# Kernel optimization log

Hardware: AMD Instinct MI355X
Metric: run time of the kernel (lower is better)

Reference implementation:

```python
import jax, jax.numpy as jnp
import numpy as np

D_IN = 1024
D_OUT = 1024
NUM_HEAD = 16
HEAD_DIM = D_OUT // NUM_HEAD
CTX = 2048


def setup_inputs() -> dict:
    key = jax.random.key(0)
    ks = jax.random.split(key, 7)
    s = 0.02
    x = jax.random.normal(ks[0], (2, CTX, D_IN), dtype=jnp.float32)
    Wq = jax.random.normal(ks[1], (D_IN, D_OUT), dtype=jnp.float32) * s
    Wk = jax.random.normal(ks[2], (D_IN, D_OUT), dtype=jnp.float32) * s
    Wv = jax.random.normal(ks[3], (D_IN, D_OUT), dtype=jnp.float32) * s
    Wo = jax.random.normal(ks[4], (D_OUT, D_OUT), dtype=jnp.float32) * s
    bo = jax.random.normal(ks[5], (D_OUT,), dtype=jnp.float32) * s
    return {"x": x, "Wq": Wq, "Wk": Wk, "Wv": Wv, "Wo": Wo, "bo": bo}


def reference(x, Wq, Wk, Wv, Wo, bo):
    B, T, _ = x.shape
    # QKV projections, split into heads: [B, H, T, hd]
    def split_heads(y):
        return y.reshape(B, T, NUM_HEAD, HEAD_DIM).transpose(0, 2, 1, 3)
    q = split_heads(x @ Wq)
    k = split_heads(x @ Wk)
    v = split_heads(x @ Wv)
    # scaled causal attention scores [B, H, T, T]
    scores = jnp.einsum("bhqd,bhkd->bhqk", q, k) / jnp.sqrt(
        jnp.asarray(HEAD_DIM, dtype=x.dtype))
    causal = jnp.tril(jnp.ones((T, T), dtype=bool))  # mask buffer triu(diag=1) -> keep lower tri
    scores = jnp.where(causal[None, None], scores, jnp.asarray(-jnp.inf, dtype=x.dtype))
    attn = jax.nn.softmax(scores, axis=-1)
    # dropout with droprate=0.0 is identity
    ctx = jnp.einsum("bhqk,bhkd->bhqd", attn, v)
    ctx = ctx.transpose(0, 2, 1, 3).reshape(B, T, D_OUT)
    return ctx @ Wo + bo
```

## Files before the change

kernel.cpp:

```cpp
#include <hip/hip_runtime.h>

typedef __bf16 bf16x8 __attribute__((ext_vector_type(8)));
typedef float f32x4 __attribute__((ext_vector_type(4)));
typedef float f32x16 __attribute__((ext_vector_type(16)));
typedef unsigned int u32x4 __attribute__((ext_vector_type(4)));

__device__ inline float bf2f(unsigned short u) {
    unsigned int x = ((unsigned int)u) << 16;
    return __builtin_bit_cast(float, x);
}
__device__ inline unsigned short f2bf(float f) {
    unsigned int x = __builtin_bit_cast(unsigned int, f);
    x += 0x7fff + ((x >> 16) & 1);
    return (unsigned short)(x >> 16);
}

__device__ __forceinline__ void gl_lds16(const unsigned short* g, unsigned short* l)
{
    __builtin_amdgcn_global_load_lds(
        (const __attribute__((address_space(1))) void*)g,
        (__attribute__((address_space(3))) void*)l, 16, 0, 0);
}

__global__ __launch_bounds__(256)
void prep(const float* __restrict__ x, unsigned short* __restrict__ xb,
          const float* __restrict__ Wq, const float* __restrict__ Wk,
          const float* __restrict__ Wv, unsigned short* __restrict__ wT)
{
    __shared__ unsigned short T[64][72];
    if (blockIdx.x < 2048) {
        const size_t i = ((size_t)blockIdx.x * 256 + threadIdx.x) * 8;
        float4 a = *reinterpret_cast<const float4*>(x + i);
        float4 b = *reinterpret_cast<const float4*>(x + i + 4);
        unsigned short t[8] = { f2bf(a.x), f2bf(a.y), f2bf(a.z), f2bf(a.w),
                                f2bf(b.x), f2bf(b.y), f2bf(b.z), f2bf(b.w) };
        *reinterpret_cast<uint4*>(xb + i) = *reinterpret_cast<uint4*>(t);
        return;
    }
    const int blk = blockIdx.x - 2048;
    const int z = blk >> 8, within = blk & 255;
    const float* W = (z == 0) ? Wq : (z == 1) ? Wk : Wv;
    unsigned short* dstBase = wT + (size_t)z * 1024 * 1024;
    const int k0 = (within >> 4) * 64, n0 = (within & 15) * 64;
    const int r = threadIdx.x >> 2, c0 = (threadIdx.x & 3) * 16;
    const float* src = W + (size_t)(k0 + r) * 1024 + n0 + c0;
    #pragma unroll
    for (int j = 0; j < 16; j += 4) {
        float4 f = *reinterpret_cast<const float4*>(src + j);
        T[r][c0 + j]     = f2bf(f.x);
        T[r][c0 + j + 1] = f2bf(f.y);
        T[r][c0 + j + 2] = f2bf(f.z);
        T[r][c0 + j + 3] = f2bf(f.w);
    }
    __syncthreads();
    unsigned short* dst = dstBase + (size_t)(n0 + r) * 1024 + k0 + c0;
    #pragma unroll
    for (int h = 0; h < 2; ++h) {
        unsigned short t8[8];
        #pragma unroll
        for (int j = 0; j < 8; ++j) t8[j] = T[c0 + h * 8 + j][r];
        *reinterpret_cast<uint4*>(dst + h * 8) = *reinterpret_cast<uint4*>(t8);
    }
}

__global__ __launch_bounds__(256)
void wconv(const float* __restrict__ W, unsigned short* __restrict__ wT)
{
    __shared__ unsigned short T[64][72];
    const int k0 = blockIdx.y * 64, n0 = blockIdx.x * 64;
    const int r = threadIdx.x >> 2, c0 = (threadIdx.x & 3) * 16;
    const float* src = W + (size_t)(k0 + r) * 1024 + n0 + c0;
    #pragma unroll
    for (int j = 0; j < 16; j += 4) {
        float4 f = *reinterpret_cast<const float4*>(src + j);
        T[r][c0 + j]     = f2bf(f.x);
        T[r][c0 + j + 1] = f2bf(f.y);
        T[r][c0 + j + 2] = f2bf(f.z);
        T[r][c0 + j + 3] = f2bf(f.w);
    }
    __syncthreads();
    unsigned short* dst = wT + (size_t)(n0 + r) * 1024 + k0 + c0;
    #pragma unroll
    for (int h = 0; h < 2; ++h) {
        unsigned short t8[8];
        #pragma unroll
        for (int j = 0; j < 8; ++j) t8[j] = T[c0 + h * 8 + j][r];
        *reinterpret_cast<uint4*>(dst + h * 8) = *reinterpret_cast<uint4*>(t8);
    }
}

template <int MODE>
__global__ __launch_bounds__(256)
void gemm128(const unsigned short* __restrict__ A,
             const unsigned short* __restrict__ BT,
             void* __restrict__ C0, void* __restrict__ C1,
             void* __restrict__ C2, const float* __restrict__ bias)
{
    __shared__ unsigned short As[128 * 32];
    __shared__ unsigned short Bs[128 * 32];

    const int tid = threadIdx.x;
    const int wave = tid >> 6, lane = tid & 63, quad = lane >> 4, l16 = lane & 15;
    const int wm = wave >> 1, wn = wave & 1;
    const int mBase = blockIdx.y * 128, nBase = blockIdx.x * 128;

    f32x4 acc[4][4] = {};

    const int srow = lane >> 2, sko = (lane & 3) * 8;

    for (int kb = 0; kb < 1024; kb += 32) {
        __syncthreads();
        #pragma unroll
        for (int j = 0; j < 2; ++j) {
            const int seg = wave * 2 + j;
            gl_lds16(A  + (size_t)(mBase + seg * 16 + srow) * 1024 + kb + sko,
                     As + seg * 512);
            gl_lds16(BT + (size_t)(nBase + seg * 16 + srow) * 1024 + kb + sko,
                     Bs + seg * 512);
        }
        __syncthreads();

        bf16x8 af[4], bf[4];
        #pragma unroll
        for (int t = 0; t < 4; ++t) {
            af[t] = *reinterpret_cast<const bf16x8*>(&As[(wm * 64 + t * 16 + l16) * 32 + quad * 8]);
            bf[t] = *reinterpret_cast<const bf16x8*>(&Bs[(wn * 64 + t * 16 + l16) * 32 + quad * 8]);
        }
        #pragma unroll
        for (int ti = 0; ti < 4; ++ti)
            #pragma unroll
            for (int tj = 0; tj < 4; ++tj)
                acc[ti][tj] = __builtin_amdgcn_mfma_f32_16x16x32_bf16(
                    af[ti], bf[tj], acc[ti][tj], 0, 0, 0);
    }

    #pragma unroll
    for (int ti = 0; ti < 4; ++ti) {
        const int row0 = mBase + wm * 64 + ti * 16 + quad * 4;
        #pragma unroll
        for (int tj = 0; tj < 4; ++tj) {
            const int col = nBase + wn * 64 + tj * 16 + l16;
            if constexpr (MODE == 0) {
                if (col < 1024) {
                    unsigned short* qb = (unsigned short*)C0;
                    #pragma unroll
                    for (int i = 0; i < 4; ++i)
                        qb[(size_t)(row0 + i) * 1024 + col] = f2bf(acc[ti][tj][i]);
                } else if (col < 2048) {
                    unsigned short* kb = (unsigned short*)C1;
                    #pragma unroll
                    for (int i = 0; i < 4; ++i)
                        kb[(size_t)(row0 + i) * 1024 + col - 1024] = f2bf(acc[ti][tj][i]);
                } else {
                    unsigned short* vT = (unsigned short*)C2;
                    unsigned short t4[4] = { f2bf(acc[ti][tj][0]), f2bf(acc[ti][tj][1]),
                                             f2bf(acc[ti][tj][2]), f2bf(acc[ti][tj][3]) };
                    *reinterpret_cast<uint2*>(&vT[(size_t)(col - 2048) * 4096 + row0]) =
                        *reinterpret_cast<uint2*>(t4);
                }
            } else {
                float* out = (float*)C0;
                const float ba = bias[col];
                #pragma unroll
                for (int i = 0; i < 4; ++i)
                    out[(size_t)(row0 + i) * 1024 + col] = acc[ti][tj][i] + ba;
            }
        }
    }
}

__global__ __launch_bounds__(256, 2)
void attn7(const unsigned short* __restrict__ q,
           const unsigned short* __restrict__ k,
           const unsigned short* __restrict__ vT,
           unsigned short* __restrict__ ctx)
{
    __shared__ unsigned short Ks[2][64 * 64];
    __shared__ unsigned short Vs[2][64 * 64];
    __shared__ float Lt[8 * 64];

    const int tid  = threadIdx.x;
    const int wave = tid >> 6, lane = tid & 63;
    const int q32 = lane & 31, hi = lane >> 5;
    const int slice = wave & 1;
    const int ks    = wave >> 1;
    const int j  = blockIdx.x;
    const int bh = blockIdx.y;
    const int b = bh >> 4, h = bh & 15;
    const int tokBase = b * 2048;
    const int colBase = h * 64;
    const int qtA = 31 - j, qtB = j;
    const int qloA = qtA * 64 + slice * 32;
    const int qloB = qtB * 64 + slice * 32;

    bf16x8 aqA[4], aqB[4];
    {
        const unsigned short* ra = q + (size_t)(tokBase + qloA + q32) * 1024 + colBase + hi * 8;
        const unsigned short* rb = q + (size_t)(tokBase + qloB + q32) * 1024 + colBase + hi * 8;
        #pragma unroll
        for (int c = 0; c < 4; ++c) {
            aqA[c] = *reinterpret_cast<const bf16x8*>(ra + c * 16);
            aqB[c] = *reinterpret_cast<const bf16x8*>(rb + c * 16);
        }
    }

    f32x16 oA[2] = {}, oB[2] = {};
    float lsA = 0.0f, lsB = 0.0f;

    const int s0 = (wave * 2 + 0) * 64 + lane;
    const int s1 = (wave * 2 + 1) * 64 + lane;
    const int r0 = s0 >> 3, sw0 = (s0 & 7) ^ (r0 & 7);
    const int r1 = s1 >> 3, sw1 = (s1 & 7) ^ (r1 & 7);
    const size_t kOff0 = (size_t)r0 * 1024 + colBase + sw0 * 8;
    const size_t kOff1 = (size_t)r1 * 1024 + colBase + sw1 * 8;
    const size_t vOff0 = (size_t)(colBase + r0) * 4096 + sw0 * 8;
    const size_t vOff1 = (size_t)(colBase + r1) * 4096 + sw1 * 8;

    auto stage = [&](int tok0, int buf) {
        gl_lds16(k  + (size_t)tok0 * 1024 + kOff0, &Ks[buf][(wave * 2 + 0) * 512]);
        gl_lds16(k  + (size_t)tok0 * 1024 + kOff1, &Ks[buf][(wave * 2 + 1) * 512]);
        gl_lds16(vT + vOff0 + tok0,                &Vs[buf][(wave * 2 + 0) * 512]);
        gl_lds16(vT + vOff1 + tok0,                &Vs[buf][(wave * 2 + 1) * 512]);
    };

    bf16x8 ak[4];
    bf16x8 bv[2][2];

    auto tile = [&](const bf16x8 (&aq)[4], f32x16 (&o)[2], float& ls,
                    int qlo, int klo) {
        if (klo > qlo + 31) return;
        f32x16 sc = (f32x16)0.0f;
        #pragma unroll
        for (int c = 0; c < 4; ++c)
            sc = __builtin_amdgcn_mfma_f32_32x32x16_bf16(ak[c], aq[c], sc, 0, 0, 0);
        float p[16];
        #pragma unroll
        for (int r = 0; r < 16; ++r) p[r] = __expf(sc[r] * 0.125f);
        if (klo + 31 > qlo) {
            #pragma unroll
            for (int r = 0; r < 16; ++r) {
                const int krow = (r & 3) + 8 * (r >> 2) + 4 * hi;
                if (klo + krow > qlo + q32) p[r] = 0.0f;
            }
        }
        #pragma unroll
        for (int r = 0; r < 16; ++r) ls += p[r];
        unsigned int pk[8];
        #pragma unroll
        for (int i = 0; i < 8; ++i)
            asm("v_cvt_pk_bf16_f32 %0, %1, %2"
                : "=v"(pk[i]) : "v"(p[2 * i]), "v"(p[2 * i + 1]));
        #pragma unroll
        for (int kc = 0; kc < 2; ++kc) {
            unsigned int x0 = pk[kc * 4 + 0], y0 = pk[kc * 4 + 2];
            unsigned int x1 = pk[kc * 4 + 1], y1 = pk[kc * 4 + 3];
            asm("v_permlane32_swap_b32 %0, %1" : "+v"(x0), "+v"(y0));
            asm("v_permlane32_swap_b32 %0, %1" : "+v"(x1), "+v"(y1));
            const u32x4 wv = { x0, x1, y0, y1 };
            const bf16x8 pa = __builtin_bit_cast(bf16x8, wv);
            #pragma unroll
            for (int dh = 0; dh < 2; ++dh)
                o[dh] = __builtin_amdgcn_mfma_f32_32x32x16_bf16(pa, bv[kc][dh], o[dh], 0, 0, 0);
        }
    };

    stage(tokBase, 0);
    __syncthreads();

    const int nkt = qtA + 1;
    int buf = 0;
    const int krowK = ks * 32 + q32;
    for (int kt = 0; kt < nkt; ++kt) {
        if (kt + 1 < nkt)
            stage(tokBase + (kt + 1) * 64, buf ^ 1);
        const unsigned short* KsB = Ks[buf];
        const unsigned short* VsB = Vs[buf];
        #pragma unroll
        for (int c = 0; c < 4; ++c) {
            const int u = c * 2 + hi;
            ak[c] = *reinterpret_cast<const bf16x8*>(
                &KsB[krowK * 64 + ((u ^ (krowK & 7)) * 8)]);
        }
        #pragma unroll
        for (int kc = 0; kc < 2; ++kc)
            #pragma unroll
            for (int dh = 0; dh < 2; ++dh) {
                const int vrow = dh * 32 + q32;
                const int u = ks * 4 + kc * 2 + hi;
                bv[kc][dh] = *reinterpret_cast<const bf16x8*>(
                    &VsB[vrow * 64 + ((u ^ (vrow & 7)) * 8)]);
            }
        const int klo = kt * 64 + ks * 32;
        tile(aqA, oA, lsA, qloA, klo);
        tile(aqB, oB, lsB, qloB, klo);
        if (kt + 1 < nkt)
            __syncthreads();
        buf ^= 1;
    }

    float* Obuf = reinterpret_cast<float*>(&Ks[0][0]);

    __syncthreads();
    Lt[(wave * 2 + 0) * 64 + lane] = lsA;
    Lt[(wave * 2 + 1) * 64 + lane] = lsB;

    auto writePartial = [&](const f32x16 (&o)[2]) {
        float* slot = Obuf + slice * 2048;
        #pragma unroll
        for (int r = 0; r < 16; ++r) {
            const int row = (r & 3) + 8 * (r >> 2) + 4 * hi;
            #pragma unroll
            for (int dh = 0; dh < 2; ++dh)
                slot[row * 64 + dh * 32 + q32] = o[dh][r];
        }
    };
    auto finalize = [&](int t, int qt, const f32x16 (&o)[2]) {
        const float lf = Lt[(slice * 2 + t) * 64 + q32]
                       + Lt[(slice * 2 + t) * 64 + 32 + q32]
                       + Lt[((slice + 2) * 2 + t) * 64 + q32]
                       + Lt[((slice + 2) * 2 + t) * 64 + 32 + q32];
        const float inv = 1.0f / lf;
        const float* slot = Obuf + slice * 2048;
        #pragma unroll
        for (int r = 0; r < 16; ++r) {
            const int row = (r & 3) + 8 * (r >> 2) + 4 * hi;
            const float invr = __shfl(inv, row);
            const size_t gr = (size_t)(tokBase + qt * 64 + slice * 32 + row) * 1024 + colBase;
            #pragma unroll
            for (int dh = 0; dh < 2; ++dh)
                ctx[gr + dh * 32 + q32] =
                    f2bf((o[dh][r] + slot[row * 64 + dh * 32 + q32]) * invr);
        }
    };

    if (ks == 1) writePartial(oA);
    __syncthreads();
    if (ks == 0) finalize(0, qtA, oA);
    __syncthreads();
    if (ks == 0) writePartial(oB);
    __syncthreads();
    if (ks == 1) finalize(1, qtB, oB);
}

extern "C" void kernel_launch(void* const* d_in, const int* in_sizes, int n_in,
                              void* d_out, int out_size, void* d_ws, size_t ws_size,
                              hipStream_t stream)
{
    const float* x  = (const float*)d_in[0];
    const float* Wq = (const float*)d_in[1];
    const float* Wk = (const float*)d_in[2];
    const float* Wv = (const float*)d_in[3];
    const float* Wo = (const float*)d_in[4];
    const float* bo = (const float*)d_in[5];
    float* out = (float*)d_out;

    unsigned short* xb     = (unsigned short*)d_ws;
    unsigned short* qb     = xb + (size_t)4096 * 1024;
    unsigned short* kb     = qb + (size_t)4096 * 1024;
    unsigned short* vT     = kb + (size_t)4096 * 1024;
    unsigned short* ctx    = xb;
    unsigned short* wqkvT  = (unsigned short*)d_out;
    unsigned short* woT    = kb;

    prep<<<2816, 256, 0, stream>>>(x, xb, Wq, Wk, Wv, wqkvT);

    gemm128<0><<<dim3(24, 32), 256, 0, stream>>>(xb, wqkvT, qb, kb, vT, nullptr);

    attn7<<<dim3(16, 32), 256, 0, stream>>>(qb, kb, vT, ctx);

    wconv<<<dim3(16, 16), 256, 0, stream>>>(Wo, woT);

    gemm128<2><<<dim3(8, 32), 256, 0, stream>>>(ctx, woT, out, nullptr, nullptr, bo);
}
```

Baseline: 183.3 us.

## Triple-buffer attention K/V staging, fold softmax scale into Q, remap blocks per XCD

The attention kernel now keeps three K/V LDS buffers with two tiles in flight. It uses explicit vmcnt waits plus a single barrier per iteration in place of two syncthreads. The 1/sqrt(d)*log2(e) scale is folded into Q during the projection GEMM epilogue so the softmax uses raw exp2. Blocks are remapped so each XCD gets a contiguous set of heads for L2 locality, and MFMA sections are wrapped in setprio. The extra buffer increases LDS use, which may affect the two-blocks-per-CU occupancy, and the hand-written vmcnt counts depend on the exact number of loads issued per stage.

```diff
diff --git a/kernel.cpp b/kernel.cpp
--- a/kernel.cpp
+++ b/kernel.cpp
@@ -5,15 +5,17 @@
 typedef float f32x16 __attribute__((ext_vector_type(16)));
 typedef unsigned int u32x4 __attribute__((ext_vector_type(4)));
 
-__device__ inline float bf2f(unsigned short u) {
-    unsigned int x = ((unsigned int)u) << 16;
-    return __builtin_bit_cast(float, x);
-}
 __device__ inline unsigned short f2bf(float f) {
     unsigned int x = __builtin_bit_cast(unsigned int, f);
     x += 0x7fff + ((x >> 16) & 1);
     return (unsigned short)(x >> 16);
 }
+
+#if __has_builtin(__builtin_amdgcn_exp2f)
+#define EXP2F(x) __builtin_amdgcn_exp2f(x)
+#else
+#define EXP2F(x) exp2f(x)
+#endif
 
 __device__ __forceinline__ void gl_lds16(const unsigned short* g, unsigned short* l)
 {
@@ -89,6 +91,8 @@
     }
 }
 
+#define QSCALE 0.18033688011112042f
+
 template <int MODE>
 __global__ __launch_bounds__(256)
 void gemm128(const unsigned short* __restrict__ A,
@@ -145,7 +149,7 @@
                     unsigned short* qb = (unsigned short*)C0;
                     #pragma unroll
                     for (int i = 0; i < 4; ++i)
-                        qb[(size_t)(row0 + i) * 1024 + col] = f2bf(acc[ti][tj][i]);
+                        qb[(size_t)(row0 + i) * 1024 + col] = f2bf(acc[ti][tj][i] * QSCALE);
                 } else if (col < 2048) {
                     unsigned short* kb = (unsigned short*)C1;
                     #pragma unroll
@@ -170,13 +174,13 @@
 }
 
 __global__ __launch_bounds__(256, 2)
-void attn7(const unsigned short* __restrict__ q,
+void attn8(const unsigned short* __restrict__ q,
            const unsigned short* __restrict__ k,
            const unsigned short* __restrict__ vT,
            unsigned short* __restrict__ ctx)
 {
-    __shared__ unsigned short Ks[2][64 * 64];
-    __shared__ unsigned short Vs[2][64 * 64];
+    __shared__ unsigned short Ks[3][64 * 64];
+    __shared__ unsigned short Vs[3][64 * 64];
     __shared__ float Lt[8 * 64];
 
     const int tid  = threadIdx.x;
@@ -184,8 +188,10 @@
     const int q32 = lane & 31, hi = lane >> 5;
     const int slice = wave & 1;
     const int ks    = wave >> 1;
-    const int j  = blockIdx.x;
-    const int bh = blockIdx.y;
+    const int L = (int)(blockIdx.x + (blockIdx.y << 4));
+    const int xcd = L & 7, idx = L >> 3;
+    const int bh = xcd * 4 + (idx >> 4);
+    const int j  = idx & 15;
     const int b = bh >> 4, h = bh & 15;
     const int tokBase = b * 2048;
     const int colBase = h * 64;
@@ -203,6 +209,9 @@
             aqB[c] = *reinterpret_cast<const bf16x8*>(rb + c * 16);
         }
     }
+    #pragma unroll
+    for (int c = 0; c < 4; ++c)
+        asm volatile("" :: "v"(aqA[c]), "v"(aqB[c]));
 
     f32x16 oA[2] = {}, oB[2] = {};
     float lsA = 0.0f, lsB = 0.0f;
@@ -230,12 +239,14 @@
                     int qlo, int klo) {
         if (klo > qlo + 31) return;
         f32x16 sc = (f32x16)0.0f;
+        __builtin_amdgcn_s_setprio(1);
         #pragma unroll
         for (int c = 0; c < 4; ++c)
             sc = __builtin_amdgcn_mfma_f32_32x32x16_bf16(ak[c], aq[c], sc, 0, 0, 0);
+        __builtin_amdgcn_s_setprio(0);
         float p[16];
         #pragma unroll
-        for (int r = 0; r < 16; ++r) p[r] = __expf(sc[r] * 0.125f);
+        for (int r = 0; r < 16; ++r) p[r] = EXP2F(sc[r]);
         if (klo + 31 > qlo) {
             #pragma unroll
             for (int r = 0; r < 16; ++r) {
@@ -258,23 +269,30 @@
             asm("v_permlane32_swap_b32 %0, %1" : "+v"(x1), "+v"(y1));
             const u32x4 wv = { x0, x1, y0, y1 };
             const bf16x8 pa = __builtin_bit_cast(bf16x8, wv);
+            __builtin_amdgcn_s_setprio(1);
             #pragma unroll
             for (int dh = 0; dh < 2; ++dh)
                 o[dh] = __builtin_amdgcn_mfma_f32_32x32x16_bf16(pa, bv[kc][dh], o[dh], 0, 0, 0);
+            __builtin_amdgcn_s_setprio(0);
         }
     };
 
+    const int nkt = qtA + 1;
     stage(tokBase, 0);
-    __syncthreads();
-
-    const int nkt = qtA + 1;
-    int buf = 0;
+    stage(tokBase + 64, 1);
+
+    int cur = 0;
     const int krowK = ks * 32 + q32;
     for (int kt = 0; kt < nkt; ++kt) {
-        if (kt + 1 < nkt)
-            stage(tokBase + (kt + 1) * 64, buf ^ 1);
-        const unsigned short* KsB = Ks[buf];
-        const unsigned short* VsB = Vs[buf];
+        if (kt + 1 < nkt) asm volatile("s_waitcnt vmcnt(4)" ::: "memory");
+        else              asm volatile("s_waitcnt vmcnt(0)" ::: "memory");
+        __builtin_amdgcn_s_barrier();
+        asm volatile("" ::: "memory");
+        const int stg = (cur == 0) ? 2 : cur - 1;
+        if (kt + 2 < nkt)
+            stage(tokBase + (kt + 2) * 64, stg);
+        const unsigned short* KsB = Ks[cur];
+        const unsigned short* VsB = Vs[cur];
         #pragma unroll
         for (int c = 0; c < 4; ++c) {
             const int u = c * 2 + hi;
@@ -293,9 +311,7 @@
         const int klo = kt * 64 + ks * 32;
         tile(aqA, oA, lsA, qloA, klo);
         tile(aqB, oB, lsB, qloB, klo);
-        if (kt + 1 < nkt)
-            __syncthreads();
-        buf ^= 1;
+        cur = (cur == 2) ? 0 : cur + 1;
     }
 
     float* Obuf = reinterpret_cast<float*>(&Ks[0][0]);
@@ -366,7 +382,7 @@
 
     gemm128<0><<<dim3(24, 32), 256, 0, stream>>>(xb, wqkvT, qb, kb, vT, nullptr);
 
-    attn7<<<dim3(16, 32), 256, 0, stream>>>(qb, kb, vT, ctx);
+    attn8<<<dim3(16, 32), 256, 0, stream>>>(qb, kb, vT, ctx);
 
     wconv<<<dim3(16, 16), 256, 0, stream>>>(Wo, woT);
 
```

After: 195.0 us. 6.4% more time.

## Replace QKV GEMM with 256x192 tile, triple-buffered, swizzled LDS kernel

Applied to the files above, without the earlier changes.

Adds a new gemm256 kernel for the fused QKV projection. It uses 512 threads with 256x192 output tiles, triple-buffered async global-to-LDS loads with explicit vmcnt waits, and an XOR-swizzled LDS layout. The larger tiles give more reuse per load, the prefetch depth is meant to hide memory latency, and the swizzle targets LDS bank conflicts. The grid becomes 256 blocks, close to the CU count, so tail effects and register pressure from 24 accumulators per wave are the risks.

```diff
diff --git a/kernel.cpp b/kernel.cpp
--- a/kernel.cpp
+++ b/kernel.cpp
@@ -5,10 +5,6 @@
 typedef float f32x16 __attribute__((ext_vector_type(16)));
 typedef unsigned int u32x4 __attribute__((ext_vector_type(4)));
 
-__device__ inline float bf2f(unsigned short u) {
-    unsigned int x = ((unsigned int)u) << 16;
-    return __builtin_bit_cast(float, x);
-}
 __device__ inline unsigned short f2bf(float f) {
     unsigned int x = __builtin_bit_cast(unsigned int, f);
     x += 0x7fff + ((x >> 16) & 1);
@@ -89,6 +85,114 @@
     }
 }
 
+__global__ __launch_bounds__(512, 2)
+void gemm256(const unsigned short* __restrict__ A,
+             const unsigned short* __restrict__ BT,
+             unsigned short* __restrict__ qb,
+             unsigned short* __restrict__ kb,
+             unsigned short* __restrict__ vT)
+{
+    __shared__ unsigned short AsB[3][256 * 32];
+    __shared__ unsigned short BsB[3][192 * 32];
+
+    const int tid  = threadIdx.x;
+    const int wave = tid >> 6, lane = tid & 63;
+    const int quad = lane >> 4, l16 = lane & 15;
+    const int wm = wave >> 2, wn = wave & 3;
+    const int mBase = blockIdx.y * 256, nBase = blockIdx.x * 192;
+
+    f32x4 acc[8][3] = {};
+
+    const int slane = lane >> 2;
+    const int su    = (lane & 3) ^ ((lane >> 4) & 3);
+    const int physq = quad ^ (l16 >> 2);
+
+    auto stage = [&](int kb0, unsigned short* As, unsigned short* Bs) {
+        #pragma unroll
+        for (int c = 0; c < 2; ++c) {
+            const int i = wave * 2 + c;
+            gl_lds16(A + (size_t)(mBase + i * 16 + slane) * 1024 + kb0 + su * 8,
+                     As + i * 512);
+        }
+        if (wave < 4) {
+            #pragma unroll
+            for (int c = 0; c < 2; ++c) {
+                const int jj = wave * 2 + c;
+                gl_lds16(BT + (size_t)(nBase + jj * 16 + slane) * 1024 + kb0 + su * 8,
+                         Bs + jj * 512);
+            }
+        } else {
+            const int jj = 8 + (wave - 4);
+            gl_lds16(BT + (size_t)(nBase + jj * 16 + slane) * 1024 + kb0 + su * 8,
+                     Bs + jj * 512);
+        }
+    };
+
+    stage(0,  AsB[0], BsB[0]);
+    stage(32, AsB[1], BsB[1]);
+
+    int cur = 0;
+    for (int t = 0; t < 32; ++t) {
+        if (t + 1 < 32) {
+            if (wave < 4) asm volatile("s_waitcnt vmcnt(4)" ::: "memory");
+            else          asm volatile("s_waitcnt vmcnt(3)" ::: "memory");
+        } else {
+            asm volatile("s_waitcnt vmcnt(0)" ::: "memory");
+        }
+        __builtin_amdgcn_s_barrier();
+        asm volatile("" ::: "memory");
+
+        const int nxt = (cur == 0) ? 2 : cur - 1;
+        if (t + 2 < 32)
+            stage((t + 2) * 32, AsB[nxt], BsB[nxt]);
+
+        const unsigned short* As = AsB[cur];
+        const unsigned short* Bs = BsB[cur];
+        bf16x8 af[8], bf[3];
+        #pragma unroll
+        for (int mr = 0; mr < 8; ++mr) {
+            const int row = wm * 128 + mr * 16 + l16;
+            af[mr] = *reinterpret_cast<const bf16x8*>(&As[row * 32 + physq * 8]);
+        }
+        #pragma unroll
+        for (int nr = 0; nr < 3; ++nr) {
+            const int row = wn * 48 + nr * 16 + l16;
+            bf[nr] = *reinterpret_cast<const bf16x8*>(&Bs[row * 32 + physq * 8]);
+        }
+        #pragma unroll
+        for (int mr = 0; mr < 8; ++mr)
+            #pragma unroll
+            for (int nr = 0; nr < 3; ++nr)
+                acc[mr][nr] = __builtin_amdgcn_mfma_f32_16x16x32_bf16(
+                    af[mr], bf[nr], acc[mr][nr], 0, 0, 0);
+
+        cur = (cur == 2) ? 0 : cur + 1;
+    }
+
+    #pragma unroll
+    for (int mr = 0; mr < 8; ++mr) {
+        const int row0 = mBase + wm * 128 + mr * 16 + quad * 4;
+        #pragma unroll
+        for (int nr = 0; nr < 3; ++nr) {
+            const int col = nBase + wn * 48 + nr * 16 + l16;
+            if (col < 1024) {
+                #pragma unroll
+                for (int i = 0; i < 4; ++i)
+                    qb[(size_t)(row0 + i) * 1024 + col] = f2bf(acc[mr][nr][i]);
+            } else if (col < 2048) {
+                #pragma unroll
+                for (int i = 0; i < 4; ++i)
+                    kb[(size_t)(row0 + i) * 1024 + col - 1024] = f2bf(acc[mr][nr][i]);
+            } else {
+                unsigned short t4[4] = { f2bf(acc[mr][nr][0]), f2bf(acc[mr][nr][1]),
+                                         f2bf(acc[mr][nr][2]), f2bf(acc[mr][nr][3]) };
+                *reinterpret_cast<uint2*>(&vT[(size_t)(col - 2048) * 4096 + row0]) =
+                    *reinterpret_cast<uint2*>(t4);
+            }
+        }
+    }
+}
+
 template <int MODE>
 __global__ __launch_bounds__(256)
 void gemm128(const unsigned short* __restrict__ A,
@@ -140,31 +244,11 @@
         #pragma unroll
         for (int tj = 0; tj < 4; ++tj) {
             const int col = nBase + wn * 64 + tj * 16 + l16;
-            if constexpr (MODE == 0) {
-                if (col < 1024) {
-                    unsigned short* qb = (unsigned short*)C0;
-                    #pragma unroll
-                    for (int i = 0; i < 4; ++i)
-                        qb[(size_t)(row0 + i) * 1024 + col] = f2bf(acc[ti][tj][i]);
-                } else if (col < 2048) {
-                    unsigned short* kb = (unsigned short*)C1;
-                    #pragma unroll
-                    for (int i = 0; i < 4; ++i)
-                        kb[(size_t)(row0 + i) * 1024 + col - 1024] = f2bf(acc[ti][tj][i]);
-                } else {
-                    unsigned short* vT = (unsigned short*)C2;
-                    unsigned short t4[4] = { f2bf(acc[ti][tj][0]), f2bf(acc[ti][tj][1]),
-                                             f2bf(acc[ti][tj][2]), f2bf(acc[ti][tj][3]) };
-                    *reinterpret_cast<uint2*>(&vT[(size_t)(col - 2048) * 4096 + row0]) =
-                        *reinterpret_cast<uint2*>(t4);
-                }
-            } else {
-                float* out = (float*)C0;
-                const float ba = bias[col];
-                #pragma unroll
-                for (int i = 0; i < 4; ++i)
-                    out[(size_t)(row0 + i) * 1024 + col] = acc[ti][tj][i] + ba;
-            }
+            float* out = (float*)C0;
+            const float ba = bias[col];
+            #pragma unroll
+            for (int i = 0; i < 4; ++i)
+                out[(size_t)(row0 + i) * 1024 + col] = acc[ti][tj][i] + ba;
         }
     }
 }
@@ -364,7 +448,7 @@
 
     prep<<<2816, 256, 0, stream>>>(x, xb, Wq, Wk, Wv, wqkvT);
 
-    gemm128<0><<<dim3(24, 32), 256, 0, stream>>>(xb, wqkvT, qb, kb, vT, nullptr);
+    gemm256<<<dim3(16, 16), 512, 0, stream>>>(xb, wqkvT, qb, kb, vT);
 
     attn7<<<dim3(16, 32), 256, 0, stream>>>(qb, kb, vT, ctx);
 
```

Measured after the change: 193.8 us. +5.7%, slower.

## Give each attention wave private K/V LDS buffers and fold softmax scale into Q

Applied to the files above, without the earlier changes.

The attention kernel now stages each wave's own 32-key K slice and V slice into per-wave LDS buffers. Completion is tracked with explicit vmcnt waits instead of block-wide __syncthreads, which removes the per-tile barrier across the four waves. The softmax scale times log2(e) is folded into the Q projection epilogue, so the inner loop uses a raw exp2 instead of multiply plus expf. Each wave now issues more global-to-LDS loads, and correctness depends on the hand-counted vmcnt values matching the outstanding loads.

```diff
diff --git a/kernel.cpp b/kernel.cpp
--- a/kernel.cpp
+++ b/kernel.cpp
@@ -5,15 +5,19 @@
 typedef float f32x16 __attribute__((ext_vector_type(16)));
 typedef unsigned int u32x4 __attribute__((ext_vector_type(4)));
 
-__device__ inline float bf2f(unsigned short u) {
-    unsigned int x = ((unsigned int)u) << 16;
-    return __builtin_bit_cast(float, x);
-}
 __device__ inline unsigned short f2bf(float f) {
     unsigned int x = __builtin_bit_cast(unsigned int, f);
     x += 0x7fff + ((x >> 16) & 1);
     return (unsigned short)(x >> 16);
 }
+
+#if __has_builtin(__builtin_amdgcn_exp2f)
+#define EXP2F(x) __builtin_amdgcn_exp2f(x)
+#else
+#define EXP2F(x) exp2f(x)
+#endif
+
+#define QSCALE 0.18033688011112042f
 
 __device__ __forceinline__ void gl_lds16(const unsigned short* g, unsigned short* l)
 {
@@ -145,7 +149,7 @@
                     unsigned short* qb = (unsigned short*)C0;
                     #pragma unroll
                     for (int i = 0; i < 4; ++i)
-                        qb[(size_t)(row0 + i) * 1024 + col] = f2bf(acc[ti][tj][i]);
+                        qb[(size_t)(row0 + i) * 1024 + col] = f2bf(acc[ti][tj][i] * QSCALE);
                 } else if (col < 2048) {
                     unsigned short* kb = (unsigned short*)C1;
                     #pragma unroll
@@ -170,13 +174,13 @@
 }
 
 __global__ __launch_bounds__(256, 2)
-void attn7(const unsigned short* __restrict__ q,
-           const unsigned short* __restrict__ k,
-           const unsigned short* __restrict__ vT,
-           unsigned short* __restrict__ ctx)
-{
-    __shared__ unsigned short Ks[2][64 * 64];
-    __shared__ unsigned short Vs[2][64 * 64];
+void attn10(const unsigned short* __restrict__ q,
+            const unsigned short* __restrict__ k,
+            const unsigned short* __restrict__ vT,
+            unsigned short* __restrict__ ctx)
+{
+    __shared__ unsigned short Kp[4][2][32 * 64];
+    __shared__ unsigned short Vp[4][2][64 * 32];
     __shared__ float Lt[8 * 64];
 
     const int tid  = threadIdx.x;
@@ -203,24 +207,32 @@
             aqB[c] = *reinterpret_cast<const bf16x8*>(rb + c * 16);
         }
     }
+    #pragma unroll
+    for (int c = 0; c < 4; ++c)
+        asm volatile("" :: "v"(aqA[c]), "v"(aqB[c]));
+    asm volatile("s_waitcnt vmcnt(0)" ::: "memory");
 
     f32x16 oA[2] = {}, oB[2] = {};
     float lsA = 0.0f, lsB = 0.0f;
 
-    const int s0 = (wave * 2 + 0) * 64 + lane;
-    const int s1 = (wave * 2 + 1) * 64 + lane;
-    const int r0 = s0 >> 3, sw0 = (s0 & 7) ^ (r0 & 7);
-    const int r1 = s1 >> 3, sw1 = (s1 & 7) ^ (r1 & 7);
-    const size_t kOff0 = (size_t)r0 * 1024 + colBase + sw0 * 8;
-    const size_t kOff1 = (size_t)r1 * 1024 + colBase + sw1 * 8;
-    const size_t vOff0 = (size_t)(colBase + r0) * 4096 + sw0 * 8;
-    const size_t vOff1 = (size_t)(colBase + r1) * 4096 + sw1 * 8;
+    const int krow_l = lane >> 3;
+    const int ku     = (lane & 7) ^ (krow_l & 7);
+    const size_t kSrc = (size_t)(ks * 32 + krow_l) * 1024 + colBase + ku * 8;
+    const int vrow_l = lane >> 2;
+    const int vu     = (lane & 3) ^ (vrow_l & 3);
+    const size_t vSrc = (size_t)(colBase + vrow_l) * 4096 + ks * 32 + vu * 8;
 
     auto stage = [&](int tok0, int buf) {
-        gl_lds16(k  + (size_t)tok0 * 1024 + kOff0, &Ks[buf][(wave * 2 + 0) * 512]);
-        gl_lds16(k  + (size_t)tok0 * 1024 + kOff1, &Ks[buf][(wave * 2 + 1) * 512]);
-        gl_lds16(vT + vOff0 + tok0,                &Vs[buf][(wave * 2 + 0) * 512]);
-        gl_lds16(vT + vOff1 + tok0,                &Vs[buf][(wave * 2 + 1) * 512]);
+        const unsigned short* kg = k + (size_t)tok0 * 1024 + kSrc;
+        unsigned short* kd = &Kp[wave][buf][0];
+        #pragma unroll
+        for (int i = 0; i < 4; ++i)
+            gl_lds16(kg + (size_t)i * 8 * 1024, kd + i * 512);
+        const unsigned short* vg = vT + (size_t)tok0 + vSrc;
+        unsigned short* vd = &Vp[wave][buf][0];
+        #pragma unroll
+        for (int i = 0; i < 4; ++i)
+            gl_lds16(vg + (size_t)i * 16 * 4096, vd + i * 512);
     };
 
     bf16x8 ak[4];
@@ -235,7 +247,7 @@
             sc = __builtin_amdgcn_mfma_f32_32x32x16_bf16(ak[c], aq[c], sc, 0, 0, 0);
         float p[16];
         #pragma unroll
-        for (int r = 0; r < 16; ++r) p[r] = __expf(sc[r] * 0.125f);
+        for (int r = 0; r < 16; ++r) p[r] = EXP2F(sc[r]);
         if (klo + 31 > qlo) {
             #pragma unroll
             for (int r = 0; r < 16; ++r) {
@@ -264,41 +276,39 @@
         }
     };
 
+    const int nkt = qtA + 1;
     stage(tokBase, 0);
-    __syncthreads();
-
-    const int nkt = qtA + 1;
+
     int buf = 0;
-    const int krowK = ks * 32 + q32;
     for (int kt = 0; kt < nkt; ++kt) {
-        if (kt + 1 < nkt)
+        if (kt + 1 < nkt) {
             stage(tokBase + (kt + 1) * 64, buf ^ 1);
-        const unsigned short* KsB = Ks[buf];
-        const unsigned short* VsB = Vs[buf];
-        #pragma unroll
-        for (int c = 0; c < 4; ++c) {
-            const int u = c * 2 + hi;
+            asm volatile("s_waitcnt vmcnt(8)" ::: "memory");
+        } else {
+            asm volatile("s_waitcnt vmcnt(0)" ::: "memory");
+        }
+
+        const unsigned short* KsB = &Kp[wave][buf][0];
+        const unsigned short* VsB = &Vp[wave][buf][0];
+        #pragma unroll
+        for (int c = 0; c < 4; ++c)
             ak[c] = *reinterpret_cast<const bf16x8*>(
-                &KsB[krowK * 64 + ((u ^ (krowK & 7)) * 8)]);
-        }
+                &KsB[q32 * 64 + (((c * 2 + hi) ^ (q32 & 7)) * 8)]);
         #pragma unroll
         for (int kc = 0; kc < 2; ++kc)
             #pragma unroll
             for (int dh = 0; dh < 2; ++dh) {
                 const int vrow = dh * 32 + q32;
-                const int u = ks * 4 + kc * 2 + hi;
                 bv[kc][dh] = *reinterpret_cast<const bf16x8*>(
-                    &VsB[vrow * 64 + ((u ^ (vrow & 7)) * 8)]);
+                    &VsB[vrow * 32 + (((kc * 2 + hi) ^ (q32 & 3)) * 8)]);
             }
         const int klo = kt * 64 + ks * 32;
         tile(aqA, oA, lsA, qloA, klo);
         tile(aqB, oB, lsB, qloB, klo);
-        if (kt + 1 < nkt)
-            __syncthreads();
         buf ^= 1;
     }
 
-    float* Obuf = reinterpret_cast<float*>(&Ks[0][0]);
+    float* Obuf = reinterpret_cast<float*>(&Kp[0][0][0]);
 
     __syncthreads();
     Lt[(wave * 2 + 0) * 64 + lane] = lsA;
@@ -366,7 +376,7 @@
 
     gemm128<0><<<dim3(24, 32), 256, 0, stream>>>(xb, wqkvT, qb, kb, vT, nullptr);
 
-    attn7<<<dim3(16, 32), 256, 0, stream>>>(qb, kb, vT, ctx);
+    attn10<<<dim3(16, 32), 256, 0, stream>>>(qb, kb, vT, ctx);
 
     wconv<<<dim3(16, 16), 256, 0, stream>>>(Wo, woT);
 
```

Measured after the change: 199.1 us. 8.6% more time.
